# Optimization experiments

Hardware: AMD Instinct MI355X
Metric: run time of the kernel (lower is better)

## Reference

```python
import jax, jax.numpy as jnp
import numpy as np

P0 = 2   # tublet_size
P = 16   # patch_size
FC = 2   # flow channels (map_x, map_y)


def patchify(x, p0, p1, p2):
    # x: (B, C, T, H, W) -> (B, (T/p0)(H/p1)(W/p2), p0*p1*p2*C)
    B, C, T, H, W = x.shape
    x = x.reshape(B, C, T // p0, p0, H // p1, p1, W // p2, p2)
    x = x.transpose(0, 2, 4, 6, 3, 5, 7, 1)  # b t h w p0 p1 p2 c
    return x.reshape(B, (T // p0) * (H // p1) * (W // p2), p0 * p1 * p2 * C)


def unpatchify(x, p0, p1, p2, C, T, H, W):
    # x: (B, N, p0*p1*p2*C) -> (B, C, T, H, W)
    B = x.shape[0]
    x = x.reshape(B, T // p0, H // p1, W // p2, p0, p1, p2, C)
    x = x.transpose(0, 7, 1, 4, 2, 5, 3, 6)  # b c t p0 h p1 w p2
    return x.reshape(B, C, T, H, W)


def bilinear_warp(imgs, mx, my):
    # imgs: (B, C, T, H, W); mx, my: (B, T, H, W) absolute sample coords.
    # Equivalent of cv2.remap INTER_LINEAR with constant (zero) border.
    B, C, T, H, W = imgs.shape
    x0 = jnp.floor(mx)
    y0 = jnp.floor(my)
    wx = (mx - x0).reshape(B, 1, T, H * W)
    wy = (my - y0).reshape(B, 1, T, H * W)
    x0i = x0.astype(jnp.int32)
    y0i = y0.astype(jnp.int32)
    imgs_flat = imgs.reshape(B, C, T, H * W)

    def gather(yi, xi):
        yc = jnp.clip(yi, 0, H - 1)
        xc = jnp.clip(xi, 0, W - 1)
        idx = (yc * W + xc).reshape(B, 1, T, H * W)
        v = jnp.take_along_axis(imgs_flat, jnp.broadcast_to(idx, (B, C, T, H * W)), axis=-1)
        valid = ((yi >= 0) & (yi <= H - 1) & (xi >= 0) & (xi <= W - 1)).reshape(B, 1, T, H * W)
        return v * valid.astype(v.dtype)

    v00 = gather(y0i, x0i)
    v01 = gather(y0i, x0i + 1)
    v10 = gather(y0i + 1, x0i)
    v11 = gather(y0i + 1, x0i + 1)
    out = (v00 * (1 - wx) * (1 - wy) + v01 * wx * (1 - wy)
           + v10 * (1 - wx) * wy + v11 * wx * wy)
    return out.reshape(B, C, T, H, W)


def setup_inputs() -> dict:
    key = jax.random.key(0)
    k1, k2, k3 = jax.random.split(key, 3)
    B, C, T, H, W = 8, 3, 16, 224, 224
    N = (T // P0) * (H // P) * (W // P)         # 1568 tokens
    D = P0 * P * P * FC                         # 1024 per-token flow dim
    output = jax.random.normal(k1, (B, N, D), dtype=jnp.float32)
    raw_target = jax.random.normal(k2, (B, C, T, H, W), dtype=jnp.float32)
    mask = jax.random.randint(k3, (B, N), 0, 2) > 0
    return {"output": output, "raw_target": raw_target, "mask": mask}


def reference(output, raw_target, mask):
    B, C, T, H, W = raw_target.shape
    # tokens -> dense flow field (B, 2, T, H, W)
    flows = unpatchify(output, P0, P, P, FC, T, H, W)
    gx = jnp.arange(W, dtype=flows.dtype)               # (W,)
    gy = jnp.arange(H, dtype=flows.dtype)[:, None]      # (H, 1)
    mx = flows[:, 0] + gx                                # (B, T, H, W)
    my = flows[:, 1] + gy
    recons = bilinear_warp(raw_target, mx, my)           # (B, C, T, H, W)
    rec_p = patchify(recons, P0, P, P)                   # (B, N, p0*p1*p2*C)
    tgt_p = patchify(raw_target, P0, P, P)
    m = mask.astype(rec_p.dtype)[..., None]              # (B, N, 1)
    diff2 = (rec_p - tgt_p) ** 2 * m
    denom = jnp.maximum(m.sum(), 1.0) * rec_p.shape[-1]
    return diff2.sum() / denom
```

## Files before the change

kernel.cpp:

```cpp
#include <hip/hip_runtime.h>

#define Bd 8
#define Cd 3
#define Td 16
#define Hd 224
#define Wd 224
#define Nd 1568
#define Dd 1024
#define HWd (Hd*Wd)
#define MASK_N (Bd*Nd)
#define PATCH_ELEMS 1536.0

#define WINP 16
#define PLANE 256
#define BUF (6*PLANE)
#define GRID_MAIN 1024
#define STG_V4 384
#define NSEG 13

struct TokGeo { int b, t2, ph, pw; };

__device__ __forceinline__ TokGeo geo(int tk) {
    TokGeo g;
    g.b = tk / Nd;
    int n = tk - g.b * Nd;
    g.t2 = n / 196;
    int rem = n - g.t2 * 196;
    g.ph = rem / 14;
    g.pw = rem - g.ph * 14;
    return g;
}

__device__ __forceinline__ int stg_goff(int j) {
    int p   = j >> 6;
    int rem = j & 63;
    int r   = rem >> 2;
    int c4  = (rem & 3) << 2;
    return (p >> 1) * (16 * HWd) + (p & 1) * HWd + r * Wd + c4;
}

__device__ __forceinline__ float compute_tok(const float* __restrict__ raw,
                                             const float* __restrict__ pl0,
                                             const TokGeo& g, int tid,
                                             float2 f0, float2 f1) {
    const int WX = g.pw << 4, WY = g.ph << 4;
    const int h = WY + (tid >> 4);
    const int w = WX + (tid & 15);

    float v00[2][3], v01[2][3], v10[2][3], v11[2][3], tg[2][3];
    float W00[2], W01[2], W10[2], W11[2];

    #pragma unroll
    for (int i0 = 0; i0 < 2; ++i0) {
        float2 f = i0 ? f1 : f0;
        float mx = f.x + (float)w;
        float my = f.y + (float)h;

        float x0 = floorf(mx), y0 = floorf(my);
        float wx = mx - x0,    wy = my - y0;
        int x0i = (int)x0, y0i = (int)y0;
        int x1i = x0i + 1, y1i = y0i + 1;

        bool vx0 = (x0i >= 0) && (x0i < Wd);
        bool vx1 = (x1i >= 0) && (x1i < Wd);
        bool vy0 = (y0i >= 0) && (y0i < Hd);
        bool vy1 = (y1i >= 0) && (y1i < Hd);

        int xc0 = min(max(x0i, 0), Wd - 1);
        int xc1 = min(max(x1i, 0), Wd - 1);
        int yc0 = min(max(y0i, 0), Hd - 1);
        int yc1 = min(max(y1i, 0), Hd - 1);

        W00[i0] = (1.f - wx) * (1.f - wy) * ((vx0 && vy0) ? 1.f : 0.f);
        W01[i0] = wx         * (1.f - wy) * ((vx1 && vy0) ? 1.f : 0.f);
        W10[i0] = (1.f - wx) * wy         * ((vx0 && vy1) ? 1.f : 0.f);
        W11[i0] = wx         * wy         * ((vx1 && vy1) ? 1.f : 0.f);

        const int lx0 = xc0 - WX, lx1 = xc1 - WX;
        const int ly0 = yc0 - WY, ly1 = yc1 - WY;
        const bool ok = (lx0 >= 0) & (lx1 < WINP) & (ly0 >= 0) & (ly1 < WINP);

        #pragma unroll
        for (int c = 0; c < Cd; ++c)
            tg[i0][c] = pl0[(((c << 1) | i0) * PLANE) + tid];

        if (ok) {
            const int b00 = (ly0 << 4) + lx0;
            const int b01 = (ly0 << 4) + lx1;
            const int b10 = (ly1 << 4) + lx0;
            const int b11 = (ly1 << 4) + lx1;
            #pragma unroll
            for (int c = 0; c < Cd; ++c) {
                const float* pl = pl0 + ((c << 1) | i0) * PLANE;
                v00[i0][c] = pl[b00];
                v01[i0][c] = pl[b01];
                v10[i0][c] = pl[b10];
                v11[i0][c] = pl[b11];
            }
        } else {
            const int i00 = yc0 * Wd + xc0;
            const int i01 = yc0 * Wd + xc1;
            const int i10 = yc1 * Wd + xc0;
            const int i11 = yc1 * Wd + xc1;
            const float* base = raw + (size_t)(g.b * 48 + (g.t2 << 1) + i0) * HWd;
            #pragma unroll
            for (int c = 0; c < Cd; ++c) {
                const float* img = base + c * (16 * HWd);
                v00[i0][c] = img[i00];
                v01[i0][c] = img[i01];
                v10[i0][c] = img[i10];
                v11[i0][c] = img[i11];
            }
        }
    }

    float acc = 0.f;
    #pragma unroll
    for (int i0 = 0; i0 < 2; ++i0) {
        #pragma unroll
        for (int c = 0; c < Cd; ++c) {
            float rec = v00[i0][c] * W00[i0] + v01[i0][c] * W01[i0]
                      + v10[i0][c] * W10[i0] + v11[i0][c] * W11[i0];
            float d = rec - tg[i0][c];
            acc += d * d;
        }
    }
    return acc;
}

__global__ void compact_kernel(const int* __restrict__ mask,
                               int* __restrict__ list,
                               int* __restrict__ bcnt) {
    const int j   = blockIdx.x;
    const int tid = threadIdx.x;
    const int i   = (j << 10) + tid;
    bool m = (i < MASK_N) && (mask[i] != 0);
    unsigned long long bal = __ballot(m);
    int lane = tid & 63, wid = tid >> 6;
    __shared__ unsigned wt[16];
    unsigned pre = (unsigned)__popcll(bal & ((1ull << lane) - 1ull));
    if (lane == 0) wt[wid] = (unsigned)__popcll(bal);
    __syncthreads();
    unsigned base = 0;
    for (int k = 0; k < wid; ++k) base += wt[k];
    if (m) list[(j << 10) + base + pre] = i;
    if (tid == 0) {
        unsigned tot = 0;
        #pragma unroll
        for (int k = 0; k < 16; ++k) tot += wt[k];
        bcnt[j] = (int)tot;
    }
}

__global__ __launch_bounds__(256)
void flow_mse_main(const float* __restrict__ outp,
                   const float* __restrict__ raw,
                   const int* __restrict__ list,
                   const int* __restrict__ bcnt,
                   float* __restrict__ partial) {
    __shared__ float lds[2 * BUF];
    __shared__ float sdata[4];
    const int tid = threadIdx.x;

    int pre1  = bcnt[0];
    int pre2  = pre1  + bcnt[1];
    int pre3  = pre2  + bcnt[2];
    int pre4  = pre3  + bcnt[3];
    int pre5  = pre4  + bcnt[4];
    int pre6  = pre5  + bcnt[5];
    int pre7  = pre6  + bcnt[6];
    int pre8  = pre7  + bcnt[7];
    int pre9  = pre8  + bcnt[8];
    int pre10 = pre9  + bcnt[9];
    int pre11 = pre10 + bcnt[10];
    int pre12 = pre11 + bcnt[11];
    const int cnt = pre12 + bcnt[12];

    #define SLOT2TK(slot, tk_out) do {                                   \
        int _s = (slot);                                                 \
        int _seg = 0, _base = 0;                                         \
        if (_s >= pre1)  { _seg = 1;  _base = pre1;  }                   \
        if (_s >= pre2)  { _seg = 2;  _base = pre2;  }                   \
        if (_s >= pre3)  { _seg = 3;  _base = pre3;  }                   \
        if (_s >= pre4)  { _seg = 4;  _base = pre4;  }                   \
        if (_s >= pre5)  { _seg = 5;  _base = pre5;  }                   \
        if (_s >= pre6)  { _seg = 6;  _base = pre6;  }                   \
        if (_s >= pre7)  { _seg = 7;  _base = pre7;  }                   \
        if (_s >= pre8)  { _seg = 8;  _base = pre8;  }                   \
        if (_s >= pre9)  { _seg = 9;  _base = pre9;  }                   \
        if (_s >= pre10) { _seg = 10; _base = pre10; }                   \
        if (_s >= pre11) { _seg = 11; _base = pre11; }                   \
        if (_s >= pre12) { _seg = 12; _base = pre12; }                   \
        (tk_out) = list[(_seg << 10) + _s - _base];                      \
    } while (0)

    const int q0 = stg_goff(tid);
    const bool k1 = tid < (STG_V4 - 256);
    const int q1 = stg_goff(k1 ? tid + 256 : 0);
    const int l0 = tid << 2;
    const int l1 = (tid << 2) + 1024;

    float4 s0, s1;
    float2 fc0, fc1, fn0, fn1;
    TokGeo gc, gn;
    float acc = 0.f;

    int idx = blockIdx.x;
    int cur = 0;

    if (idx < cnt) {
        int tk; SLOT2TK(idx, tk);
        gc = geo(tk);
        const float* base = raw + (size_t)(gc.b * 48 + (gc.t2 << 1)) * HWd
                          + (gc.ph << 4) * Wd + (gc.pw << 4);
        s0 = *(const float4*)(base + q0);
        if (k1) s1 = *(const float4*)(base + q1);
        const float2* fp = (const float2*)(outp + ((size_t)tk << 10));
        fc0 = fp[tid]; fc1 = fp[256 + tid];
        *(float4*)(lds + l0) = s0;
        if (k1) *(float4*)(lds + l1) = s1;
    }

    while (idx < cnt) {
        int nidx = idx + GRID_MAIN;
        __syncthreads();
        bool have_next = nidx < cnt;
        if (have_next) {
            int ntk; SLOT2TK(nidx, ntk);
            gn = geo(ntk);
            const float* base = raw + (size_t)(gn.b * 48 + (gn.t2 << 1)) * HWd
                              + (gn.ph << 4) * Wd + (gn.pw << 4);
            s0 = *(const float4*)(base + q0);
            if (k1) s1 = *(const float4*)(base + q1);
            const float2* fp = (const float2*)(outp + ((size_t)ntk << 10));
            fn0 = fp[tid]; fn1 = fp[256 + tid];
        }
        acc += compute_tok(raw, lds + cur * BUF, gc, tid, fc0, fc1);
        if (have_next) {
            float* dst = lds + (cur ^ 1) * BUF;
            *(float4*)(dst + l0) = s0;
            if (k1) *(float4*)(dst + l1) = s1;
        }
        idx = nidx; cur ^= 1;
        gc = gn; fc0 = fn0; fc1 = fn1;
    }

    for (int off = 32; off > 0; off >>= 1) acc += __shfl_down(acc, off, 64);
    if ((tid & 63) == 0) sdata[tid >> 6] = acc;
    __syncthreads();
    if (tid == 0)
        partial[blockIdx.x] = sdata[0] + sdata[1] + sdata[2] + sdata[3];
    #undef SLOT2TK
}

__global__ void finalize_kernel(const float* __restrict__ partial,
                                const int* __restrict__ bcnt,
                                float* __restrict__ out) {
    double s = 0.0;
    for (int i = threadIdx.x; i < GRID_MAIN; i += blockDim.x)
        s += (double)partial[i];
    for (int off = 32; off > 0; off >>= 1)
        s += __shfl_down(s, off, 64);
    __shared__ double sdat[4];
    int lane = threadIdx.x & 63, wid = threadIdx.x >> 6;
    if (lane == 0) sdat[wid] = s;
    __syncthreads();
    if (threadIdx.x == 0) {
        double st = sdat[0] + sdat[1] + sdat[2] + sdat[3];
        int ct = 0;
        #pragma unroll
        for (int k = 0; k < NSEG; ++k) ct += bcnt[k];
        double denom = (double)(ct > 0 ? ct : 1) * PATCH_ELEMS;
        out[0] = (float)(st / denom);
    }
}

extern "C" void kernel_launch(void* const* d_in, const int* in_sizes, int n_in,
                              void* d_out, int out_size, void* d_ws, size_t ws_size,
                              hipStream_t stream) {
    const float* outp = (const float*)d_in[0];
    const float* raw  = (const float*)d_in[1];
    const int*   mask = (const int*)d_in[2];
    float* out = (float*)d_out;

    int*   bcnt    = (int*)d_ws;
    float* partial = (float*)((char*)d_ws + 64);
    int*   list    = (int*)((char*)d_ws + 64 + GRID_MAIN * 4);

    compact_kernel<<<NSEG, 1024, 0, stream>>>(mask, list, bcnt);
    flow_mse_main<<<GRID_MAIN, 256, 0, stream>>>(outp, raw, list, bcnt, partial);
    finalize_kernel<<<1, 256, 0, stream>>>(partial, bcnt, out);
}
```

Before: 156.1 us.

## Process full-width strip per block with halo LDS tile and in-block mask

Replaces the compaction kernel and per-token gather scheme with one block per (batch, frame, patch-row) strip. Each block stages a 20-row, full-width tile (16 rows plus a 2-row halo) of all channels into LDS, reads the 14 mask bits itself, and loops over the masked patches in that strip. This removes a kernel launch and the slot-to-token search, reuses one staged tile across neighbouring patches, and lets small flows that cross patch borders hit LDS instead of global memory. The cost is that every strip's raw rows are loaded even when few or none of its patches are masked, and each block uses more LDS, which limits how many blocks can share a compute unit.

```diff
diff --git a/kernel.cpp b/kernel.cpp
--- a/kernel.cpp
+++ b/kernel.cpp
@@ -6,270 +6,186 @@
 #define Hd 224
 #define Wd 224
 #define Nd 1568
-#define Dd 1024
 #define HWd (Hd*Wd)
-#define MASK_N (Bd*Nd)
+#define NPH 14
+#define NPW 14
+#define NT2 8
+#define NSTRIP (Bd*NT2*NPH)
+#define GRID_MAIN (NSTRIP*2)
+#define HALO 2
+#define SROWS (16 + 2*HALO)
+#define LROW 232
+#define LPLANE (SROWS*LROW)
+#define LDS_FLOATS (Cd*LPLANE)
+#define STG_TOTAL (Cd*SROWS*56)
 #define PATCH_ELEMS 1536.0
 
-#define WINP 16
-#define PLANE 256
-#define BUF (6*PLANE)
-#define GRID_MAIN 1024
-#define STG_V4 384
-#define NSEG 13
-
-struct TokGeo { int b, t2, ph, pw; };
-
-__device__ __forceinline__ TokGeo geo(int tk) {
-    TokGeo g;
-    g.b = tk / Nd;
-    int n = tk - g.b * Nd;
-    g.t2 = n / 196;
-    int rem = n - g.t2 * 196;
-    g.ph = rem / 14;
-    g.pw = rem - g.ph * 14;
-    return g;
+__global__ __launch_bounds__(256)
+void flow_mse_strip(const float* __restrict__ outp,
+                    const float* __restrict__ raw,
+                    const int* __restrict__ mask,
+                    float* __restrict__ partial,
+                    int* __restrict__ scnt) {
+    __shared__ float lds[LDS_FLOATS];
+    __shared__ unsigned smask;
+    __shared__ float sred[4];
+
+    const int tid   = threadIdx.x;
+    const int bid   = blockIdx.x;
+    const int strip = bid >> 1;
+    const int i0    = bid & 1;
+    const int b     = strip / (NT2 * NPH);
+    const int sr    = strip - b * (NT2 * NPH);
+    const int t2    = sr / NPH;
+    const int ph    = sr - t2 * NPH;
+    const int t     = (t2 << 1) | i0;
+    const int ybase = (ph << 4) - HALO;
+
+    float4 rbuf[14];
+    #pragma unroll
+    for (int it = 0; it < 14; ++it) {
+        int v = tid + (it << 8);
+        if (v < STG_TOTAL) {
+            int c    = v / 1120;
+            int rem  = v - c * 1120;
+            int j    = rem / 56;
+            int col4 = rem - j * 56;
+            int y    = ybase + j;
+            int yc   = min(max(y, 0), Hd - 1);
+            const float* g = raw + ((size_t)(b * Cd + c) * Td + t) * HWd
+                           + yc * Wd + (col4 << 2);
+            rbuf[it] = *(const float4*)g;
+        }
+    }
+
+    const int nbase = t2 * 196 + ph * NPW;
+    bool mm = false;
+    if (tid < NPW) mm = (mask[b * Nd + nbase + tid] != 0);
+    unsigned long long bal = __ballot(mm);
+    if (tid == 0) smask = (unsigned)(bal & 0x3FFFull);
+
+    #pragma unroll
+    for (int it = 0; it < 14; ++it) {
+        int v = tid + (it << 8);
+        if (v < STG_TOTAL) {
+            int c    = v / 1120;
+            int rem  = v - c * 1120;
+            int j    = rem / 56;
+            int col4 = rem - j * 56;
+            *(float4*)(lds + (c * SROWS + j) * LROW + (col4 << 2)) = rbuf[it];
+        }
+    }
+    __syncthreads();
+
+    unsigned mw = smask;
+    float acc = 0.f;
+    const int py = tid >> 4, px = tid & 15;
+    const int h  = (ph << 4) + py;
+
+    if (mw) {
+        int pw = __ffs((int)mw) - 1;
+        const float* fpf = outp + (((size_t)(b * Nd + nbase + pw)) << 10) + (i0 << 9);
+        float2 f = ((const float2*)fpf)[tid];
+
+        while (1) {
+            unsigned nmw = mw & (mw - 1);
+            int npw = 0;
+            float2 nf = make_float2(0.f, 0.f);
+            if (nmw) {
+                npw = __ffs((int)nmw) - 1;
+                const float* nfp = outp + (((size_t)(b * Nd + nbase + npw)) << 10) + (i0 << 9);
+                nf = ((const float2*)nfp)[tid];
+            }
+
+            {
+                const int w = (pw << 4) + px;
+                float mx = f.x + (float)w;
+                float my = f.y + (float)h;
+                float x0 = floorf(mx), y0 = floorf(my);
+                float wx = mx - x0,    wy = my - y0;
+                int x0i = (int)x0, y0i = (int)y0;
+                int x1i = x0i + 1,  y1i = y0i + 1;
+
+                bool vx0 = (x0i >= 0) && (x0i < Wd);
+                bool vx1 = (x1i >= 0) && (x1i < Wd);
+                bool vy0 = (y0i >= 0) && (y0i < Hd);
+                bool vy1 = (y1i >= 0) && (y1i < Hd);
+
+                float W00 = (1.f - wx) * (1.f - wy) * ((vx0 && vy0) ? 1.f : 0.f);
+                float W01 = wx         * (1.f - wy) * ((vx1 && vy0) ? 1.f : 0.f);
+                float W10 = (1.f - wx) * wy         * ((vx0 && vy1) ? 1.f : 0.f);
+                float W11 = wx         * wy         * ((vx1 && vy1) ? 1.f : 0.f);
+
+                int xc0 = min(max(x0i, 0), Wd - 1);
+                int xc1 = min(max(x1i, 0), Wd - 1);
+                int yc0 = min(max(y0i, 0), Hd - 1);
+                int yc1 = min(max(y1i, 0), Hd - 1);
+                int ly0 = yc0 - ybase, ly1 = yc1 - ybase;
+                const int bt = (py + HALO) * LROW + w;
+
+                if ((ly0 >= 0) & (ly1 < SROWS)) {
+                    const int b00 = ly0 * LROW + xc0;
+                    const int b01 = ly0 * LROW + xc1;
+                    const int b10 = ly1 * LROW + xc0;
+                    const int b11 = ly1 * LROW + xc1;
+                    #pragma unroll
+                    for (int c = 0; c < Cd; ++c) {
+                        const float* pl = lds + c * LPLANE;
+                        float rec = pl[b00] * W00 + pl[b01] * W01
+                                  + pl[b10] * W10 + pl[b11] * W11;
+                        float d = rec - pl[bt];
+                        acc += d * d;
+                    }
+                } else {
+                    const int i00 = yc0 * Wd + xc0;
+                    const int i01 = yc0 * Wd + xc1;
+                    const int i10 = yc1 * Wd + xc0;
+                    const int i11 = yc1 * Wd + xc1;
+                    #pragma unroll
+                    for (int c = 0; c < Cd; ++c) {
+                        const float* img = raw + ((size_t)(b * Cd + c) * Td + t) * HWd;
+                        float rec = img[i00] * W00 + img[i01] * W01
+                                  + img[i10] * W10 + img[i11] * W11;
+                        float d = rec - (lds + c * LPLANE)[bt];
+                        acc += d * d;
+                    }
+                }
+            }
+
+            if (!nmw) break;
+            mw = nmw; pw = npw; f = nf;
+        }
+    }
+
+    for (int off = 32; off > 0; off >>= 1) acc += __shfl_down(acc, off, 64);
+    if ((tid & 63) == 0) sred[tid >> 6] = acc;
+    __syncthreads();
+    if (tid == 0) {
+        partial[bid] = sred[0] + sred[1] + sred[2] + sred[3];
+        if (i0 == 0) scnt[strip] = __popc(smask);
+    }
 }
 
-__device__ __forceinline__ int stg_goff(int j) {
-    int p   = j >> 6;
-    int rem = j & 63;
-    int r   = rem >> 2;
-    int c4  = (rem & 3) << 2;
-    return (p >> 1) * (16 * HWd) + (p & 1) * HWd + r * Wd + c4;
-}
-
-__device__ __forceinline__ float compute_tok(const float* __restrict__ raw,
-                                             const float* __restrict__ pl0,
-                                             const TokGeo& g, int tid,
-                                             float2 f0, float2 f1) {
-    const int WX = g.pw << 4, WY = g.ph << 4;
-    const int h = WY + (tid >> 4);
-    const int w = WX + (tid & 15);
-
-    float v00[2][3], v01[2][3], v10[2][3], v11[2][3], tg[2][3];
-    float W00[2], W01[2], W10[2], W11[2];
-
-    #pragma unroll
-    for (int i0 = 0; i0 < 2; ++i0) {
-        float2 f = i0 ? f1 : f0;
-        float mx = f.x + (float)w;
-        float my = f.y + (float)h;
-
-        float x0 = floorf(mx), y0 = floorf(my);
-        float wx = mx - x0,    wy = my - y0;
-        int x0i = (int)x0, y0i = (int)y0;
-        int x1i = x0i + 1, y1i = y0i + 1;
-
-        bool vx0 = (x0i >= 0) && (x0i < Wd);
-        bool vx1 = (x1i >= 0) && (x1i < Wd);
-        bool vy0 = (y0i >= 0) && (y0i < Hd);
-        bool vy1 = (y1i >= 0) && (y1i < Hd);
-
-        int xc0 = min(max(x0i, 0), Wd - 1);
-        int xc1 = min(max(x1i, 0), Wd - 1);
-        int yc0 = min(max(y0i, 0), Hd - 1);
-        int yc1 = min(max(y1i, 0), Hd - 1);
-
-        W00[i0] = (1.f - wx) * (1.f - wy) * ((vx0 && vy0) ? 1.f : 0.f);
-        W01[i0] = wx         * (1.f - wy) * ((vx1 && vy0) ? 1.f : 0.f);
-        W10[i0] = (1.f - wx) * wy         * ((vx0 && vy1) ? 1.f : 0.f);
-        W11[i0] = wx         * wy         * ((vx1 && vy1) ? 1.f : 0.f);
-
-        const int lx0 = xc0 - WX, lx1 = xc1 - WX;
-        const int ly0 = yc0 - WY, ly1 = yc1 - WY;
-        const bool ok = (lx0 >= 0) & (lx1 < WINP) & (ly0 >= 0) & (ly1 < WINP);
-
-        #pragma unroll
-        for (int c = 0; c < Cd; ++c)
-            tg[i0][c] = pl0[(((c << 1) | i0) * PLANE) + tid];
-
-        if (ok) {
-            const int b00 = (ly0 << 4) + lx0;
-            const int b01 = (ly0 << 4) + lx1;
-            const int b10 = (ly1 << 4) + lx0;
-            const int b11 = (ly1 << 4) + lx1;
-            #pragma unroll
-            for (int c = 0; c < Cd; ++c) {
-                const float* pl = pl0 + ((c << 1) | i0) * PLANE;
-                v00[i0][c] = pl[b00];
-                v01[i0][c] = pl[b01];
-                v10[i0][c] = pl[b10];
-                v11[i0][c] = pl[b11];
-            }
-        } else {
-            const int i00 = yc0 * Wd + xc0;
-            const int i01 = yc0 * Wd + xc1;
-            const int i10 = yc1 * Wd + xc0;
-            const int i11 = yc1 * Wd + xc1;
-            const float* base = raw + (size_t)(g.b * 48 + (g.t2 << 1) + i0) * HWd;
-            #pragma unroll
-            for (int c = 0; c < Cd; ++c) {
-                const float* img = base + c * (16 * HWd);
-                v00[i0][c] = img[i00];
-                v01[i0][c] = img[i01];
-                v10[i0][c] = img[i10];
-                v11[i0][c] = img[i11];
-            }
-        }
-    }
-
-    float acc = 0.f;
-    #pragma unroll
-    for (int i0 = 0; i0 < 2; ++i0) {
-        #pragma unroll
-        for (int c = 0; c < Cd; ++c) {
-            float rec = v00[i0][c] * W00[i0] + v01[i0][c] * W01[i0]
-                      + v10[i0][c] * W10[i0] + v11[i0][c] * W11[i0];
-            float d = rec - tg[i0][c];
-            acc += d * d;
-        }
-    }
-    return acc;
-}
-
-__global__ void compact_kernel(const int* __restrict__ mask,
-                               int* __restrict__ list,
-                               int* __restrict__ bcnt) {
-    const int j   = blockIdx.x;
+__global__ void finalize_kernel(const float* __restrict__ partial,
+                                const int* __restrict__ scnt,
+                                float* __restrict__ out) {
     const int tid = threadIdx.x;
-    const int i   = (j << 10) + tid;
-    bool m = (i < MASK_N) && (mask[i] != 0);
-    unsigned long long bal = __ballot(m);
+    double s = 0.0;
+    for (int i = tid; i < GRID_MAIN; i += 256) s += (double)partial[i];
+    int c = 0;
+    for (int i = tid; i < NSTRIP; i += 256) c += scnt[i];
+    for (int off = 32; off > 0; off >>= 1) {
+        s += __shfl_down(s, off, 64);
+        c += __shfl_down(c, off, 64);
+    }
+    __shared__ double sd[4];
+    __shared__ int    sc[4];
     int lane = tid & 63, wid = tid >> 6;
-    __shared__ unsigned wt[16];
-    unsigned pre = (unsigned)__popcll(bal & ((1ull << lane) - 1ull));
-    if (lane == 0) wt[wid] = (unsigned)__popcll(bal);
+    if (lane == 0) { sd[wid] = s; sc[wid] = c; }
     __syncthreads();
-    unsigned base = 0;
-    for (int k = 0; k < wid; ++k) base += wt[k];
-    if (m) list[(j << 10) + base + pre] = i;
     if (tid == 0) {
-        unsigned tot = 0;
-        #pragma unroll
-        for (int k = 0; k < 16; ++k) tot += wt[k];
-        bcnt[j] = (int)tot;
-    }
-}
-
-__global__ __launch_bounds__(256)
-void flow_mse_main(const float* __restrict__ outp,
-                   const float* __restrict__ raw,
-                   const int* __restrict__ list,
-                   const int* __restrict__ bcnt,
-                   float* __restrict__ partial) {
-    __shared__ float lds[2 * BUF];
-    __shared__ float sdata[4];
-    const int tid = threadIdx.x;
-
-    int pre1  = bcnt[0];
-    int pre2  = pre1  + bcnt[1];
-    int pre3  = pre2  + bcnt[2];
-    int pre4  = pre3  + bcnt[3];
-    int pre5  = pre4  + bcnt[4];
-    int pre6  = pre5  + bcnt[5];
-    int pre7  = pre6  + bcnt[6];
-    int pre8  = pre7  + bcnt[7];
-    int pre9  = pre8  + bcnt[8];
-    int pre10 = pre9  + bcnt[9];
-    int pre11 = pre10 + bcnt[10];
-    int pre12 = pre11 + bcnt[11];
-    const int cnt = pre12 + bcnt[12];
-
-    #define SLOT2TK(slot, tk_out) do {                                   \
-        int _s = (slot);                                                 \
-        int _seg = 0, _base = 0;                                         \
-        if (_s >= pre1)  { _seg = 1;  _base = pre1;  }                   \
-        if (_s >= pre2)  { _seg = 2;  _base = pre2;  }                   \
-        if (_s >= pre3)  { _seg = 3;  _base = pre3;  }                   \
-        if (_s >= pre4)  { _seg = 4;  _base = pre4;  }                   \
-        if (_s >= pre5)  { _seg = 5;  _base = pre5;  }                   \
-        if (_s >= pre6)  { _seg = 6;  _base = pre6;  }                   \
-        if (_s >= pre7)  { _seg = 7;  _base = pre7;  }                   \
-        if (_s >= pre8)  { _seg = 8;  _base = pre8;  }                   \
-        if (_s >= pre9)  { _seg = 9;  _base = pre9;  }                   \
-        if (_s >= pre10) { _seg = 10; _base = pre10; }                   \
-        if (_s >= pre11) { _seg = 11; _base = pre11; }                   \
-        if (_s >= pre12) { _seg = 12; _base = pre12; }                   \
-        (tk_out) = list[(_seg << 10) + _s - _base];                      \
-    } while (0)
-
-    const int q0 = stg_goff(tid);
-    const bool k1 = tid < (STG_V4 - 256);
-    const int q1 = stg_goff(k1 ? tid + 256 : 0);
-    const int l0 = tid << 2;
-    const int l1 = (tid << 2) + 1024;
-
-    float4 s0, s1;
-    float2 fc0, fc1, fn0, fn1;
-    TokGeo gc, gn;
-    float acc = 0.f;
-
-    int idx = blockIdx.x;
-    int cur = 0;
-
-    if (idx < cnt) {
-        int tk; SLOT2TK(idx, tk);
-        gc = geo(tk);
-        const float* base = raw + (size_t)(gc.b * 48 + (gc.t2 << 1)) * HWd
-                          + (gc.ph << 4) * Wd + (gc.pw << 4);
-        s0 = *(const float4*)(base + q0);
-        if (k1) s1 = *(const float4*)(base + q1);
-        const float2* fp = (const float2*)(outp + ((size_t)tk << 10));
-        fc0 = fp[tid]; fc1 = fp[256 + tid];
-        *(float4*)(lds + l0) = s0;
-        if (k1) *(float4*)(lds + l1) = s1;
-    }
-
-    while (idx < cnt) {
-        int nidx = idx + GRID_MAIN;
-        __syncthreads();
-        bool have_next = nidx < cnt;
-        if (have_next) {
-            int ntk; SLOT2TK(nidx, ntk);
-            gn = geo(ntk);
-            const float* base = raw + (size_t)(gn.b * 48 + (gn.t2 << 1)) * HWd
-                              + (gn.ph << 4) * Wd + (gn.pw << 4);
-            s0 = *(const float4*)(base + q0);
-            if (k1) s1 = *(const float4*)(base + q1);
-            const float2* fp = (const float2*)(outp + ((size_t)ntk << 10));
-            fn0 = fp[tid]; fn1 = fp[256 + tid];
-        }
-        acc += compute_tok(raw, lds + cur * BUF, gc, tid, fc0, fc1);
-        if (have_next) {
-            float* dst = lds + (cur ^ 1) * BUF;
-            *(float4*)(dst + l0) = s0;
-            if (k1) *(float4*)(dst + l1) = s1;
-        }
-        idx = nidx; cur ^= 1;
-        gc = gn; fc0 = fn0; fc1 = fn1;
-    }
-
-    for (int off = 32; off > 0; off >>= 1) acc += __shfl_down(acc, off, 64);
-    if ((tid & 63) == 0) sdata[tid >> 6] = acc;
-    __syncthreads();
-    if (tid == 0)
-        partial[blockIdx.x] = sdata[0] + sdata[1] + sdata[2] + sdata[3];
-    #undef SLOT2TK
-}
-
-__global__ void finalize_kernel(const float* __restrict__ partial,
-                                const int* __restrict__ bcnt,
-                                float* __restrict__ out) {
-    double s = 0.0;
-    for (int i = threadIdx.x; i < GRID_MAIN; i += blockDim.x)
-        s += (double)partial[i];
-    for (int off = 32; off > 0; off >>= 1)
-        s += __shfl_down(s, off, 64);
-    __shared__ double sdat[4];
-    int lane = threadIdx.x & 63, wid = threadIdx.x >> 6;
-    if (lane == 0) sdat[wid] = s;
-    __syncthreads();
-    if (threadIdx.x == 0) {
-        double st = sdat[0] + sdat[1] + sdat[2] + sdat[3];
-        int ct = 0;
-        #pragma unroll
-        for (int k = 0; k < NSEG; ++k) ct += bcnt[k];
+        double st = sd[0] + sd[1] + sd[2] + sd[3];
+        int    ct = sc[0] + sc[1] + sc[2] + sc[3];
         double denom = (double)(ct > 0 ? ct : 1) * PATCH_ELEMS;
         out[0] = (float)(st / denom);
     }
@@ -283,11 +199,9 @@
     const int*   mask = (const int*)d_in[2];
     float* out = (float*)d_out;
 
-    int*   bcnt    = (int*)d_ws;
-    float* partial = (float*)((char*)d_ws + 64);
-    int*   list    = (int*)((char*)d_ws + 64 + GRID_MAIN * 4);
-
-    compact_kernel<<<NSEG, 1024, 0, stream>>>(mask, list, bcnt);
-    flow_mse_main<<<GRID_MAIN, 256, 0, stream>>>(outp, raw, list, bcnt, partial);
-    finalize_kernel<<<1, 256, 0, stream>>>(partial, bcnt, out);
+    float* partial = (float*)d_ws;
+    int*   scnt    = (int*)((char*)d_ws + GRID_MAIN * 4);
+
+    flow_mse_strip<<<GRID_MAIN, 256, 0, stream>>>(outp, raw, mask, partial, scnt);
+    finalize_kernel<<<1, 256, 0, stream>>>(partial, scnt, out);
 }
```

After: 200.8 us. 1.29x slower.
